# Performance work log

Hardware: AMD Instinct MI355X
Metric: run time of the kernel (lower is better)

The kernel has to match this reference:

```python
import jax, jax.numpy as jnp
import numpy as np

B, N_H, N = 32, 16, 64
R, REP, NUM_CLS = 1024, 1024, 117
NUM_ITER = 2
T_LIS, K_LIS, W_LIS = 8.3, 12.0, 10.0

# static pair indices: x in [0,n_h), y in [0,n), x != y  -> M = N_H*N - N_H
_xx, _yy = np.meshgrid(np.arange(N_H), np.arange(N), indexing='ij')
_mask = _xx != _yy
X_IDX = jnp.asarray(_xx[_mask], dtype=jnp.int32)  # [M]
Y_IDX = jnp.asarray(_yy[_mask], dtype=jnp.int32)  # [M]
M = int(_mask.sum())


def lis(x):
    # low-grade suppression
    return T_LIS / (1.0 + jnp.exp(K_LIS - W_LIS * x))


def setup_inputs() -> dict:
    key = jax.random.key(0)
    ks = jax.random.split(key, 18)
    s = 0.02
    p = lambda k, shp: (jax.random.normal(k, shp) * s).astype(jnp.float32)
    box_features = jax.random.normal(ks[0], (B, N, R), dtype=jnp.float32)
    box_coords = jax.random.uniform(ks[1], (B, N, 4), dtype=jnp.float32)
    box_labels = jax.random.randint(ks[2], (B, N), 0, NUM_CLS).astype(jnp.int32)
    box_labels = box_labels.at[:, :N_H].set(0)  # first N_H are humans (human_idx=0)
    box_scores = jax.random.uniform(ks[3], (B, N), dtype=jnp.float32)
    return {
        'box_features': box_features, 'box_coords': box_coords,
        'box_labels': box_labels, 'box_scores': box_scores,
        'W1': p(ks[4], (2 * R, REP)), 'b1': jnp.zeros((REP,), jnp.float32),
        'W2': p(ks[5], (REP, REP // 2)), 'b2': jnp.zeros((REP // 2,), jnp.float32),
        'W3': p(ks[6], (REP // 2, 1)), 'b3': jnp.zeros((1,), jnp.float32),
        'Ws': p(ks[7], (R, REP)), 'bs': jnp.zeros((REP,), jnp.float32),
        'Wo': p(ks[8], (R, REP)), 'bo': jnp.zeros((REP,), jnp.float32),
        'Wsu': p(ks[9], (R + REP, R)),
        'Wou': p(ks[10], (R + REP, R)),
    }


def reference(box_features, box_coords, box_labels, box_scores,
              W1, b1, W2, b2, W3, b3, Ws, bs, Wo, bo, Wsu, Wou):
    def per_image(enc, coords, labels, scores):
        # enc: [N, R]
        A = jnp.zeros((N_H, N), enc.dtype)
        for _ in range(NUM_ITER):
            pe = jnp.concatenate([enc[X_IDX], enc[Y_IDX]], axis=1)  # [M, 2R]
            h = jax.nn.relu(pe @ W1 + b1)
            h = jax.nn.relu(h @ W2 + b2)
            w = (h @ W3 + b3)[:, 0]  # [M]
            A = jnp.zeros((N_H, N), enc.dtype).at[X_IDX, Y_IDX].set(jax.nn.sigmoid(w))
            msg_h = A @ jax.nn.relu(enc @ Wo + bo)                      # [N_H, REP]
            enc_h = jnp.concatenate([enc[:N_H], msg_h], axis=1) @ Wsu  # [N_H, R]
            enc = enc.at[:N_H].set(enc_h)
            msg_o = A.T @ jax.nn.relu(enc_h @ Ws + bs)                  # [N, REP]
            enc = jnp.concatenate([enc, msg_o], axis=1) @ Wou           # [N, R]
        pair = jnp.concatenate([enc[X_IDX], enc[Y_IDX]], axis=1)  # [M, 2R]
        prod = lis(scores[X_IDX]) * lis(scores[Y_IDX])            # [M]
        # identity object_class_to_target_class: class c -> [c]
        prior = jnp.zeros((M, NUM_CLS), enc.dtype).at[jnp.arange(M), labels[Y_IDX]].set(prod)
        prior = A[X_IDX, Y_IDX][:, None] * prior
        return pair, coords[X_IDX], coords[Y_IDX], prior

    pair, bh, bo_, prior = jax.vmap(per_image)(box_features, box_coords, box_labels, box_scores)
    return (pair.reshape(B * M, 2 * R), bh, bo_, prior.reshape(B * M, NUM_CLS))
```

## Files before the change

kernel.cpp:

```cpp
#include <hip/hip_runtime.h>

#define B_   32
#define N_   64
#define NH   16
#define R_   1024
#define REP  1024
#define M_   1008
#define BM   (B_ * M_)
#define NCLS 117

#define MD_DIRECT 0
#define MD_CC1    2

typedef short bhalf8 __attribute__((ext_vector_type(8)));
typedef float f32x4  __attribute__((ext_vector_type(4)));

typedef __attribute__((address_space(3))) void       lds_t;
typedef const __attribute__((address_space(1))) void gbl_t;
__device__ __forceinline__ void gld16(const void* g, void* l)
{
    __builtin_amdgcn_global_load_lds((gbl_t*)g, (lds_t*)l, 16, 0, 0);
}

__device__ __forceinline__ int xcd_swz(int orig, int q)
{
    return (orig & 7) * q + (orig >> 3);
}

__device__ __forceinline__ unsigned short f2bf(float f)
{
    union { float f; unsigned int u; } x; x.f = f;
    unsigned int r = x.u + 0x7FFFu + ((x.u >> 16) & 1u);
    return (unsigned short)(r >> 16);
}
__device__ __forceinline__ float bf2f(unsigned short u)
{
    union { unsigned int i; float f; } x; x.i = ((unsigned int)u) << 16; return x.f;
}

__device__ __forceinline__ unsigned int addrelu2(unsigned int a, unsigned int b)
{
    union { unsigned int u; float f; } la, ha, lb, hb;
    la.u = a << 16;          ha.u = a & 0xffff0000u;
    lb.u = b << 16;          hb.u = b & 0xffff0000u;
    float lo = fmaxf(la.f + lb.f, 0.f);
    float hi = fmaxf(ha.f + hb.f, 0.f);
    unsigned int r;
    asm("v_cvt_pk_bf16_f32 %0, %1, %2" : "=v"(r) : "v"(lo), "v"(hi));
    return r;
}

__device__ __forceinline__ void wait_vm(int n)
{
    if (n >= 8)      asm volatile("s_waitcnt vmcnt(8)" ::: "memory");
    else if (n == 6) asm volatile("s_waitcnt vmcnt(6)" ::: "memory");
    else if (n == 4) asm volatile("s_waitcnt vmcnt(4)" ::: "memory");
    else if (n == 3) asm volatile("s_waitcnt vmcnt(3)" ::: "memory");
    else if (n == 2) asm volatile("s_waitcnt vmcnt(2)" ::: "memory");
    else             asm volatile("s_waitcnt vmcnt(0)" ::: "memory");
}
__device__ __forceinline__ void wait_vm_lgkm(int n)
{
    if (n >= 12)      asm volatile("s_waitcnt vmcnt(12) lgkmcnt(0)" ::: "memory");
    else if (n >= 10) asm volatile("s_waitcnt vmcnt(10) lgkmcnt(0)" ::: "memory");
    else              asm volatile("s_waitcnt vmcnt(8) lgkmcnt(0)" ::: "memory");
}

__device__ __forceinline__ void tr32(const float* in, unsigned short* out,
                                     int K, int N, int local)
{
    __shared__ float t[32][33];
    int kb = K >> 5;
    int k0 = (local % kb) * 32, n0 = (local / kb) * 32;
    int tx = threadIdx.x & 31, ty = threadIdx.x >> 5;
#pragma unroll
    for (int r = 0; r < 4; ++r)
        t[ty + r * 8][tx] = in[(size_t)(k0 + ty + r * 8) * N + n0 + tx];
    __syncthreads();
#pragma unroll
    for (int r = 0; r < 4; ++r)
        out[(size_t)(n0 + ty + r * 8) * K + k0 + tx] = f2bf(t[tx][ty + r * 8]);
}

__global__ __launch_bounds__(256)
void prep_all(const float* __restrict__ W1, const float* __restrict__ W2,
              const float* __restrict__ Wo, const float* __restrict__ Ws,
              const float* __restrict__ Wsu, const float* __restrict__ Wou,
              const float* __restrict__ bo_, const float* __restrict__ b1_,
              const float* __restrict__ feat,
              unsigned short* __restrict__ Wfused, unsigned short* __restrict__ W2t,
              unsigned short* __restrict__ Wst, unsigned short* __restrict__ Wsut,
              unsigned short* __restrict__ Wout, float* __restrict__ biasFull,
              unsigned short* __restrict__ enc0bf)
{
    int bx = blockIdx.x;
    if      (bx < 1024) tr32(W1 + 1024 * 1024, Wfused,               1024, 1024, bx);
    else if (bx < 2048) tr32(Wo,               Wfused + 1024 * 1024, 1024, 1024, bx - 1024);
    else if (bx < 3072) tr32(W1,               Wfused + 2048 * 1024, 1024, 1024, bx - 2048);
    else if (bx < 3584) tr32(W2,  W2t,  1024, 512,  bx - 3072);
    else if (bx < 4608) tr32(Ws,  Wst,  1024, 1024, bx - 3584);
    else if (bx < 6656) tr32(Wsu, Wsut, 2048, 1024, bx - 4608);
    else if (bx < 8704) tr32(Wou, Wout, 2048, 1024, bx - 6656);
    else if (bx < 8716) {
        int c = (bx - 8704) * 256 + threadIdx.x;
        float v = 0.f;
        if (c >= 2048)      v = b1_[c - 2048];
        else if (c >= 1024) v = bo_[c - 1024];
        biasFull[c] = v;
    } else {
        int i = (bx - 8716) * 256 + threadIdx.x;
        float4 a = ((const float4*)feat)[2 * i];
        float4 b = ((const float4*)feat)[2 * i + 1];
        uint4 o;
        o.x = (unsigned)f2bf(a.x) | ((unsigned)f2bf(a.y) << 16);
        o.y = (unsigned)f2bf(a.z) | ((unsigned)f2bf(a.w) << 16);
        o.z = (unsigned)f2bf(b.x) | ((unsigned)f2bf(b.y) << 16);
        o.w = (unsigned)f2bf(b.z) | ((unsigned)f2bf(b.w) << 16);
        ((uint4*)enc0bf)[i] = o;
    }
}

__global__ __launch_bounds__(256)
void gemm_uvgo(const unsigned short* __restrict__ enc,
               const unsigned short* __restrict__ Wf,
               const float* __restrict__ biasFull, unsigned short* __restrict__ XX)
{
    __shared__ unsigned short As[3][128 * 32];
    __shared__ unsigned short Bs[3][128 * 32];
    const int tid  = threadIdx.x;
    const int lane = tid & 63, wave = tid >> 6;
    const int wm = wave & 1, wn = wave >> 1;
    const int l15 = lane & 15, lk = lane >> 4;
    const int wgid = xcd_swz(blockIdx.x, 48);
    const int row0 = (wgid & 15) * 128, col0 = (wgid >> 4) * 128;
    const int kq = (lane & 3) * 8;

    const unsigned short* pA[2];
    const unsigned short* pB[2];
    int ldsOff[2];
#pragma unroll
    for (int i = 0; i < 2; ++i) {
        int tr = wave * 32 + (lane >> 2) + i * 16;
        pA[i]  = enc + (size_t)(row0 + tr) * 1024 + kq;
        pB[i]  = Wf  + (size_t)(col0 + tr) * 1024 + kq;
        ldsOff[i] = wave * 1024 + i * 512 + lane * 8;
    }

#define STG_UV(slot, k0) do {                          \
        gld16(pA[0] + (k0), &As[slot][ldsOff[0]]);     \
        gld16(pA[1] + (k0), &As[slot][ldsOff[1]]);     \
        gld16(pB[0] + (k0), &Bs[slot][ldsOff[0]]);     \
        gld16(pB[1] + (k0), &Bs[slot][ldsOff[1]]); } while (0)

    f32x4 acc[4][4];
#pragma unroll
    for (int i = 0; i < 4; ++i)
#pragma unroll
    for (int j = 0; j < 4; ++j) acc[i][j] = (f32x4)0.f;

    STG_UV(0, 0);
    STG_UV(1, 32);
    for (int t = 0; t < 32; ++t) {
        const int slot = t % 3;
        if (t + 2 < 32) STG_UV((t + 2) % 3, (t + 2) * 32);
        wait_vm(t < 30 ? 8 : (t == 30 ? 4 : 0));
        __builtin_amdgcn_s_barrier();
        __builtin_amdgcn_sched_barrier(0);
        bhalf8 af[4], bf4[4];
#pragma unroll
        for (int mt = 0; mt < 4; ++mt)
            af[mt] = *(bhalf8*)&As[slot][(wm * 64 + mt * 16 + l15) * 32 + lk * 8];
#pragma unroll
        for (int nt = 0; nt < 4; ++nt)
            bf4[nt] = *(bhalf8*)&Bs[slot][(wn * 64 + nt * 16 + l15) * 32 + lk * 8];
#pragma unroll
        for (int mt = 0; mt < 4; ++mt)
#pragma unroll
        for (int nt = 0; nt < 4; ++nt)
            acc[mt][nt] = __builtin_amdgcn_mfma_f32_16x16x32_bf16(af[mt], bf4[nt],
                                                                  acc[mt][nt], 0, 0, 0);
        __builtin_amdgcn_sched_barrier(0);
        __builtin_amdgcn_s_barrier();
    }
#undef STG_UV

#pragma unroll
    for (int mt = 0; mt < 4; ++mt)
#pragma unroll
    for (int r = 0; r < 4; ++r) {
        int row = row0 + wm * 64 + mt * 16 + lk * 4 + r;
#pragma unroll
        for (int nt = 0; nt < 4; ++nt) {
            int col = col0 + wn * 64 + nt * 16 + l15;
            float v = acc[mt][nt][r] + biasFull[col];
            if ((col >> 10) == 1) v = fmaxf(v, 0.f);
            XX[(size_t)row * 3072 + col] = f2bf(v);
        }
    }
}

__global__ __launch_bounds__(256)
void pair_bf(const unsigned short* __restrict__ XX,
             const unsigned short* __restrict__ W2t, const float* __restrict__ b2,
             const float* __restrict__ W3f, float* __restrict__ wpart)
{
    __shared__ unsigned short As[128 * 32];
    __shared__ unsigned short Bs[3][128 * 32];
    __shared__ float red[2][128];
    const int tid  = threadIdx.x;
    const int lane = tid & 63, wave = tid >> 6;
    const int wm = wave & 1, wn = wave >> 1;
    const int l15 = lane & 15, lk = lane >> 4;
    const int wgid = xcd_swz(blockIdx.x, 126);
    const int cx = wgid & 3, ry = wgid >> 2;
    const int row0 = ry * 128, col0 = cx * 128;

    const int srow = tid >> 1, skh = tid & 1;
    int rg = row0 + srow;
    int b  = rg / M_, m = rg % M_;
    int x  = m / 63, jj = m % 63;
    int y  = jj + (jj >= x ? 1 : 0);
    const unsigned short* Up = XX + ((size_t)(b * 64 + x)) * 3072 + 2048 + skh * 16;
    const unsigned short* Vp = XX + ((size_t)(b * 64 + y)) * 3072 + skh * 16;
    unsigned short* AsW = As + srow * 32 + skh * 16;

    const int kq = (lane & 3) * 8;
    const unsigned short* pB[2];
    int bO[2];
#pragma unroll
    for (int i = 0; i < 2; ++i) {
        int tr = wave * 32 + (lane >> 2) + i * 16;
        pB[i] = W2t + (size_t)(col0 + tr) * REP + kq;
        bO[i] = wave * 1024 + i * 512 + lane * 8;
    }

#define STG_B(slot, k0) do {                        \
        gld16(pB[0] + (k0), &Bs[slot][bO[0]]);      \
        gld16(pB[1] + (k0), &Bs[slot][bO[1]]); } while (0)

    f32x4 acc[4][4];
#pragma unroll
    for (int i = 0; i < 4; ++i)
#pragma unroll
    for (int j = 0; j < 4; ++j) acc[i][j] = (f32x4)0.f;

    uint4 cu0 = *(const uint4*)(Up);
    uint4 cu1 = *(const uint4*)(Up + 8);
    uint4 cv0 = *(const uint4*)(Vp);
    uint4 cv1 = *(const uint4*)(Vp + 8);
    STG_B(0, 0);
    STG_B(1, 32);

    for (int t = 0; t < 32; ++t) {
        const int slot = t % 3;
        const int kn = (t + 1 < 32) ? (t + 1) * 32 : 0;
        uint4 nu0 = *(const uint4*)(Up + kn);
        uint4 nu1 = *(const uint4*)(Up + kn + 8);
        uint4 nv0 = *(const uint4*)(Vp + kn);
        uint4 nv1 = *(const uint4*)(Vp + kn + 8);
        if (t + 2 < 32) STG_B((t + 2) % 3, (t + 2) * 32);

        uint4 h0, h1;
        h0.x = addrelu2(cu0.x, cv0.x); h0.y = addrelu2(cu0.y, cv0.y);
        h0.z = addrelu2(cu0.z, cv0.z); h0.w = addrelu2(cu0.w, cv0.w);
        h1.x = addrelu2(cu1.x, cv1.x); h1.y = addrelu2(cu1.y, cv1.y);
        h1.z = addrelu2(cu1.z, cv1.z); h1.w = addrelu2(cu1.w, cv1.w);
        *(uint4*)(AsW)     = h0;
        *(uint4*)(AsW + 8) = h1;

        wait_vm_lgkm(t == 0 ? 8 : (t < 30 ? 12 : (t == 30 ? 10 : 8)));
        __builtin_amdgcn_s_barrier();
        __builtin_amdgcn_sched_barrier(0);
        bhalf8 af[4], bf4[4];
#pragma unroll
        for (int mt = 0; mt < 4; ++mt)
            af[mt] = *(bhalf8*)&As[(wm * 64 + mt * 16 + l15) * 32 + lk * 8];
#pragma unroll
        for (int nt = 0; nt < 4; ++nt)
            bf4[nt] = *(bhalf8*)&Bs[slot][(wn * 64 + nt * 16 + l15) * 32 + lk * 8];
#pragma unroll
        for (int mt = 0; mt < 4; ++mt)
#pragma unroll
        for (int nt = 0; nt < 4; ++nt)
            acc[mt][nt] = __builtin_amdgcn_mfma_f32_16x16x32_bf16(af[mt], bf4[nt],
                                                                  acc[mt][nt], 0, 0, 0);
        __builtin_amdgcn_sched_barrier(0);
        __builtin_amdgcn_s_barrier();
        cu0 = nu0; cu1 = nu1; cv0 = nv0; cv1 = nv1;
    }
#undef STG_B

    float b2v[4], w3v[4];
#pragma unroll
    for (int nt = 0; nt < 4; ++nt) {
        int col = col0 + wn * 64 + nt * 16 + l15;
        b2v[nt] = b2[col];
        w3v[nt] = W3f[col];
    }
#pragma unroll
    for (int mt = 0; mt < 4; ++mt)
#pragma unroll
    for (int r = 0; r < 4; ++r) {
        int rloc = wm * 64 + mt * 16 + lk * 4 + r;
        float p = 0.f;
#pragma unroll
        for (int nt = 0; nt < 4; ++nt)
            p += fmaxf(acc[mt][nt][r] + b2v[nt], 0.f) * w3v[nt];
        p += __shfl_xor(p, 1); p += __shfl_xor(p, 2);
        p += __shfl_xor(p, 4); p += __shfl_xor(p, 8);
        if (l15 == 0) red[wn][rloc] = p;
    }
    __syncthreads();
    if (tid < 128)
        wpart[cx * BM + row0 + tid] = red[0][tid] + red[1][tid];
}

__device__ __forceinline__ void compute_A(const float* __restrict__ wpart, float b3v,
                                          int b, float* Al, int t)
{
    for (int i = t; i < NH * N_; i += 128) {
        int y = i & 63, x = i >> 6;
        float v = 0.f;
        if (y != x) {
            int j = y - (y > x ? 1 : 0);
            int r = b * M_ + x * 63 + j;
            float s = b3v + wpart[r] + wpart[BM + r] + wpart[2 * BM + r] + wpart[3 * BM + r];
            v = 1.f / (1.f + expf(-s));
        }
        Al[i] = v;
    }
}

__global__ __launch_bounds__(128)
void msgh_kernel(const float* __restrict__ wpart, const float* __restrict__ b3,
                 const unsigned short* __restrict__ XX,
                 unsigned short* __restrict__ msgh)
{
    __shared__ float Al[NH * N_];
    __shared__ float Gl[N_][128];
    const int wgid = xcd_swz(blockIdx.x, 32);
    int b = wgid >> 3, c0 = (wgid & 7) * 128, t = threadIdx.x;
    compute_A(wpart, b3[0], b, Al, t);
    for (int y = 0; y < N_; ++y)
        Gl[y][t] = bf2f(XX[((size_t)(b * 64 + y)) * 3072 + 1024 + c0 + t]);
    __syncthreads();
    for (int x = 0; x < NH; ++x) {
        float s = 0.f;
#pragma unroll 8
        for (int y = 0; y < N_; ++y) s += Al[x * N_ + y] * Gl[y][t];
        msgh[((size_t)(b * NH + x)) * REP + c0 + t] = f2bf(s);
    }
}

__global__ __launch_bounds__(256)
void gemm_small(const unsigned short* __restrict__ A1, const unsigned short* __restrict__ A2,
                const unsigned short* __restrict__ Bt, const float* __restrict__ bias,
                unsigned short* __restrict__ Cb, int K, int Nc, int doRelu, int mode)
{
    __shared__ unsigned short As[4][64 * 32];
    __shared__ unsigned short Bs[4][64 * 32];
    const int tid  = threadIdx.x;
    const int lane = tid & 63, wave = tid >> 6;
    const int wr = wave & 1, wc = wave >> 1;
    const int l15 = lane & 15, lk = lane >> 4;
    const int wgid = xcd_swz(blockIdx.x, 16);
    const int row0 = (wgid & 7) * 64, col0 = (wgid >> 3) * 64;
    const int kq = (lane & 3) * 8;

    int tr = wave * 16 + (lane >> 2);
    int rr = row0 + tr;
    const unsigned short* p1;
    const unsigned short* p2 = nullptr;
    if (mode == MD_DIRECT) {
        p1 = A1 + (size_t)rr * K;
    } else {
        int b = rr >> 4, x = rr & 15;
        p1 = A1 + (size_t)(b * 64 + x) * 1024;
        p2 = A2 + (size_t)rr * 1024 - 1024;
    }
    const unsigned short* pA1 = p1 + kq;
    const unsigned short* pA2 = p2 ? p2 + kq : nullptr;
    const unsigned short* pB  = Bt + (size_t)(col0 + tr) * K + kq;
    const int stO = wave * 512 + lane * 8;
    const int kSw = (mode != MD_DIRECT) ? 1024 : K;
    const int NT = K >> 5;

#define STG_MID(slot, k0) do {                                  \
        const unsigned short* ap = ((k0) < kSw) ? pA1 : pA2;    \
        gld16(ap + (k0), &As[slot][stO]);                       \
        gld16(pB + (k0), &Bs[slot][stO]); } while (0)

    f32x4 acc[2][2];
#pragma unroll
    for (int i = 0; i < 2; ++i)
#pragma unroll
    for (int j = 0; j < 2; ++j) acc[i][j] = (f32x4)0.f;

    STG_MID(0, 0);
    STG_MID(1, 32);
    STG_MID(2, 64);
    for (int t = 0; t < NT; ++t) {
        const int slot = t & 3;
        if (t + 3 < NT) STG_MID((t + 3) & 3, (t + 3) * 32);
        int rem = NT - 1 - t;
        wait_vm(rem >= 3 ? 6 : rem * 2);
        __builtin_amdgcn_s_barrier();
        __builtin_amdgcn_sched_barrier(0);
        bhalf8 af[2], bf4[2];
#pragma unroll
        for (int mt = 0; mt < 2; ++mt)
            af[mt] = *(bhalf8*)&As[slot][(wr * 32 + mt * 16 + l15) * 32 + lk * 8];
#pragma unroll
        for (int nt = 0; nt < 2; ++nt)
            bf4[nt] = *(bhalf8*)&Bs[slot][(wc * 32 + nt * 16 + l15) * 32 + lk * 8];
#pragma unroll
        for (int mt = 0; mt < 2; ++mt)
#pragma unroll
        for (int nt = 0; nt < 2; ++nt)
            acc[mt][nt] = __builtin_amdgcn_mfma_f32_16x16x32_bf16(af[mt], bf4[nt],
                                                                  acc[mt][nt], 0, 0, 0);
        __builtin_amdgcn_sched_barrier(0);
        __builtin_amdgcn_s_barrier();
    }
#undef STG_MID

#pragma unroll
    for (int mt = 0; mt < 2; ++mt)
#pragma unroll
    for (int r = 0; r < 4; ++r) {
        int row = row0 + wr * 32 + mt * 16 + lk * 4 + r;
#pragma unroll
        for (int nt = 0; nt < 2; ++nt) {
            int col = col0 + wc * 32 + nt * 16 + l15;
            float v = acc[mt][nt][r];
            if (bias) v += bias[col];
            if (doRelu) v = fmaxf(v, 0.f);
            Cb[(size_t)row * Nc + col] = f2bf(v);
        }
    }
}

__global__ __launch_bounds__(256)
void gemm_cc2(const unsigned short* __restrict__ enc,
              const unsigned short* __restrict__ ench,
              const unsigned short* __restrict__ Gs,
              const unsigned short* __restrict__ Wout,
              const float* __restrict__ wpart, const float* __restrict__ b3,
              float* __restrict__ Cf, unsigned short* __restrict__ Cb)
{
    __shared__ unsigned short As[3][64 * 32];
    __shared__ unsigned short Bt[3][64 * 32];
    __shared__ unsigned short Bb[3][64 * 32];
    __shared__ unsigned short GsL[16][1056];
    __shared__ float Al[16][64];
    __shared__ float gsl[16][68];

    const int tid  = threadIdx.x;
    const int lane = tid & 63, wave = tid >> 6;
    const int wr = wave & 1, wc = wave >> 1;
    const int l15 = lane & 15, lk = lane >> 4;
    const int wgid = xcd_swz(blockIdx.x, 64);
    const int b = wgid >> 4, col0 = (wgid & 15) * 64;
    const int kq = (lane & 3) * 8;

#pragma unroll
    for (int j = 0; j < 8; ++j) {
        int idx = j * 256 + tid;
        int row = idx >> 7, c8 = (idx & 127) * 8;
        uint4 v = *(const uint4*)(Gs + ((size_t)(b * 16 + row)) * 1024 + c8);
        *(uint4*)&GsL[row][c8] = v;
    }
    float b3v = b3[0];
#pragma unroll
    for (int j = 0; j < 4; ++j) {
        int i = j * 256 + tid;
        int y = i & 63, x = i >> 6;
        float v = 0.f;
        if (y != x) {
            int jj = y - (y > x ? 1 : 0);
            int r = b * M_ + x * 63 + jj;
            float s = b3v + wpart[r] + wpart[BM + r] + wpart[2 * BM + r] + wpart[3 * BM + r];
            v = 1.f / (1.f + expf(-s));
        }
        Al[x][y] = v;
    }
    asm volatile("s_waitcnt lgkmcnt(0)" ::: "memory");

    int tr = wave * 16 + (lane >> 2);
    const unsigned short* pA = (tr < 16 ? ench + ((size_t)(b * 16 + tr)) * 1024
                                        : enc  + ((size_t)(b * 64 + tr)) * 1024) + kq;
    const unsigned short* pBt = Wout + (size_t)(col0 + tr) * 2048 + kq;
    const unsigned short* pBb = pBt + 1024;
    const int stO = wave * 512 + lane * 8;

#define STG_C2(slot, k0) do {                      \
        gld16(pA  + (k0), &As[slot][stO]);         \
        gld16(pBt + (k0), &Bt[slot][stO]);         \
        gld16(pBb + (k0), &Bb[slot][stO]); } while (0)

    f32x4 acc[2][2];
    f32x4 accg[2];
#pragma unroll
    for (int i = 0; i < 2; ++i) {
        accg[i] = (f32x4)0.f;
#pragma unroll
        for (int j = 0; j < 2; ++j) acc[i][j] = (f32x4)0.f;
    }

    STG_C2(0, 0);
    STG_C2(1, 32);
    for (int t = 0; t < 32; ++t) {
        const int slot = t % 3;
        if (t + 2 < 32) STG_C2((t + 2) % 3, (t + 2) * 32);
        wait_vm(t < 30 ? 6 : (t == 30 ? 3 : 0));
        __builtin_amdgcn_s_barrier();
        __builtin_amdgcn_sched_barrier(0);
        bhalf8 af[2], bt4[2], bb4[2], ags;
#pragma unroll
        for (int mt = 0; mt < 2; ++mt)
            af[mt] = *(bhalf8*)&As[slot][(wr * 32 + mt * 16 + l15) * 32 + lk * 8];
#pragma unroll
        for (int nt = 0; nt < 2; ++nt) {
            bt4[nt] = *(bhalf8*)&Bt[slot][(wc * 32 + nt * 16 + l15) * 32 + lk * 8];
            bb4[nt] = *(bhalf8*)&Bb[slot][(wc * 32 + nt * 16 + l15) * 32 + lk * 8];
        }
        ags = *(bhalf8*)&GsL[l15][t * 32 + lk * 8];
#pragma unroll
        for (int mt = 0; mt < 2; ++mt)
#pragma unroll
        for (int nt = 0; nt < 2; ++nt)
            acc[mt][nt] = __builtin_amdgcn_mfma_f32_16x16x32_bf16(af[mt], bt4[nt],
                                                                  acc[mt][nt], 0, 0, 0);
#pragma unroll
        for (int nt = 0; nt < 2; ++nt)
            accg[nt] = __builtin_amdgcn_mfma_f32_16x16x32_bf16(ags, bb4[nt],
                                                               accg[nt], 0, 0, 0);
        __builtin_amdgcn_sched_barrier(0);
        __builtin_amdgcn_s_barrier();
    }
#undef STG_C2

    if (wr == 0) {
#pragma unroll
        for (int nt = 0; nt < 2; ++nt)
#pragma unroll
        for (int r = 0; r < 4; ++r)
            gsl[lk * 4 + r][wc * 32 + nt * 16 + l15] = accg[nt][r];
    }
    __syncthreads();

#pragma unroll
    for (int x = 0; x < 16; ++x) {
        float g0 = gsl[x][wc * 32 + l15];
        float g1 = gsl[x][wc * 32 + 16 + l15];
#pragma unroll
        for (int mt = 0; mt < 2; ++mt)
#pragma unroll
        for (int r = 0; r < 4; ++r) {
            float a = Al[x][wr * 32 + mt * 16 + lk * 4 + r];
            acc[mt][0][r] += a * g0;
            acc[mt][1][r] += a * g1;
        }
    }
#pragma unroll
    for (int mt = 0; mt < 2; ++mt)
#pragma unroll
    for (int r = 0; r < 4; ++r) {
        size_t row = (size_t)b * 64 + wr * 32 + mt * 16 + lk * 4 + r;
#pragma unroll
        for (int nt = 0; nt < 2; ++nt) {
            int col = col0 + wc * 32 + nt * 16 + l15;
            float v = acc[mt][nt][r];
            if (Cf) Cf[row * 1024 + col] = v;
            else    Cb[row * 1024 + col] = f2bf(v);
        }
    }
}

__device__ __forceinline__ float lis_f(float x)
{
    return 8.3f / (1.f + expf(12.f - 10.f * x));
}

__global__ __launch_bounds__(256)
void outputs_all(const float* __restrict__ enc, const float* __restrict__ coords,
                 const float* __restrict__ wpart, const float* __restrict__ b3,
                 const int* __restrict__ labels, const float* __restrict__ scores,
                 float* __restrict__ out0, float* __restrict__ out1,
                 float* __restrict__ out2, float* __restrict__ out3)
{
    int bx = blockIdx.x;
    if (bx < 64512) {
        int i = bx * 256 + threadIdx.x;
        int r = i >> 9, q = i & 511;
        int b = r / M_, m = r % M_;
        int x = m / 63, j = m % 63;
        int y = j + (j >= x ? 1 : 0);
        const float4* e4 = (const float4*)enc;
        float4 v = (q < 256) ? e4[(b * 64 + x) * 256 + q]
                             : e4[(b * 64 + y) * 256 + (q - 256)];
        ((float4*)out0)[i] = v;
    } else if (bx < 64638) {
        int r = (bx - 64512) * 256 + threadIdx.x;
        int b = r / M_, m = r % M_;
        int x = m / 63, j = m % 63;
        int y = j + (j >= x ? 1 : 0);
        const float4* c4 = (const float4*)coords;
        ((float4*)out1)[r] = c4[b * 64 + x];
        ((float4*)out2)[r] = c4[b * 64 + y];
    } else {
        int i = (bx - 64638) * 256 + threadIdx.x;
        int r = i / NCLS, c = i % NCLS;
        int b = r / M_, m = r % M_;
        int x = m / 63, j = m % 63;
        int y = j + (j >= x ? 1 : 0);
        int lab = labels[b * 64 + y];
        float val = 0.f;
        if (c == lab) {
            float w = b3[0] + wpart[r] + wpart[BM + r] + wpart[2 * BM + r] + wpart[3 * BM + r];
            float A = 1.f / (1.f + expf(-w));
            float sx = scores[b * 64 + x], sy = scores[b * 64 + y];
            val = A * lis_f(sx) * lis_f(sy);
        }
        out3[i] = val;
    }
}

extern "C" void kernel_launch(void* const* d_in, const int* in_sizes, int n_in,
                              void* d_out, int out_size, void* d_ws, size_t ws_size,
                              hipStream_t stream)
{
    const float* box_features = (const float*)d_in[0];
    const float* box_coords   = (const float*)d_in[1];
    const int*   box_labels   = (const int*)d_in[2];
    const float* box_scores   = (const float*)d_in[3];
    const float* W1  = (const float*)d_in[4];
    const float* b1  = (const float*)d_in[5];
    const float* W2  = (const float*)d_in[6];
    const float* b2  = (const float*)d_in[7];
    const float* W3  = (const float*)d_in[8];
    const float* b3  = (const float*)d_in[9];
    const float* Ws  = (const float*)d_in[10];
    const float* bs  = (const float*)d_in[11];
    const float* Wo  = (const float*)d_in[12];
    const float* bo  = (const float*)d_in[13];
    const float* Wsu = (const float*)d_in[14];
    const float* Wou = (const float*)d_in[15];

    float* wsf  = (float*)d_ws;
    float* encA = wsf;           wsf += (size_t)B_ * N_ * R_;
    float* wpart= wsf;           wsf += (size_t)4 * BM;
    float* biasFull = wsf;       wsf += 3072;

    unsigned short* wsu = (unsigned short*)wsf;
    unsigned short* enc0bf = wsu;  wsu += (size_t)B_ * N_ * R_;
    unsigned short* encIbf = wsu;  wsu += (size_t)B_ * N_ * R_;
    unsigned short* XX     = wsu;  wsu += (size_t)B_ * N_ * 3072;
    unsigned short* msghbf = wsu;  wsu += (size_t)B_ * NH * REP;
    unsigned short* enchbf = wsu;  wsu += (size_t)B_ * NH * R_;
    unsigned short* Gsbf   = wsu;  wsu += (size_t)B_ * NH * REP;
    unsigned short* Wfused = wsu;  wsu += (size_t)3072 * 1024;
    unsigned short* W2t    = wsu;  wsu += (size_t)512 * 1024;
    unsigned short* Wst    = wsu;  wsu += (size_t)1024 * 1024;
    unsigned short* Wsut   = wsu;  wsu += (size_t)1024 * 2048;
    unsigned short* Wout   = wsu;  wsu += (size_t)1024 * 2048;

    float* out0 = (float*)d_out;
    float* out1 = out0 + (size_t)BM * 2048;
    float* out2 = out1 + (size_t)BM * 4;
    float* out3 = out2 + (size_t)BM * 4;

    prep_all<<<9740, 256, 0, stream>>>(W1, W2, Wo, Ws, Wsu, Wou, bo, b1, box_features,
                                       Wfused, W2t, Wst, Wsut, Wout, biasFull, enc0bf);

    for (int it = 0; it < 2; ++it) {
        const unsigned short* enc = (it == 0) ? enc0bf : encIbf;
        gemm_uvgo<<<384, 256, 0, stream>>>(enc, Wfused, biasFull, XX);
        pair_bf<<<1008, 256, 0, stream>>>(XX, W2t, b2, W3, wpart);
        msgh_kernel<<<256, 128, 0, stream>>>(wpart, b3, XX, msghbf);
        gemm_small<<<128, 256, 0, stream>>>(enc, msghbf, Wsut, nullptr,
                                            enchbf, 2048, 1024, 0, MD_CC1);
        gemm_small<<<128, 256, 0, stream>>>(enchbf, nullptr, Wst, bs,
                                            Gsbf, 1024, 1024, 1, MD_DIRECT);
        gemm_cc2<<<512, 256, 0, stream>>>(enc, enchbf, Gsbf, Wout, wpart, b3,
                                          (it == 1) ? encA : nullptr,
                                          (it == 0) ? encIbf : nullptr);
    }

    outputs_all<<<79380, 256, 0, stream>>>(encA, box_coords, wpart, b3,
                                           box_labels, box_scores,
                                           out0, out1, out2, out3);
}
```

Baseline: 709.8 us.

## Widen pair_bf tiles to full 512 columns, removing split-N partial sums

The pair MLP kernel now has each 512-thread workgroup compute all 512 hidden columns for 128 pair rows, instead of four workgroups each covering 128 columns. The relu(U+V) A-tile is then built once per row block rather than four times, and the four-way wpart partial-sum buffer and its summation in the consumer kernels go away. The trade-off is a larger LDS footprint (about 96KB for B staging), more accumulator registers per thread, and only 252 workgroups, which could lower occupancy and make pipelining less effective on 256 CUs. The XCD swizzle is generalized to handle 252 blocks not dividing evenly by 8.

```diff
diff --git a/kernel.cpp b/kernel.cpp
--- a/kernel.cpp
+++ b/kernel.cpp
@@ -26,6 +26,11 @@
 {
     return (orig & 7) * q + (orig >> 3);
 }
+__device__ __forceinline__ int xcd_swz_gen(int orig, int q, int r)
+{
+    int x = orig & 7, o = orig >> 3;
+    return (x < r ? x * (q + 1) : r * (q + 1) + (x - r) * q) + o;
+}
 
 __device__ __forceinline__ unsigned short f2bf(float f)
 {
@@ -61,9 +66,10 @@
 }
 __device__ __forceinline__ void wait_vm_lgkm(int n)
 {
-    if (n >= 12)      asm volatile("s_waitcnt vmcnt(12) lgkmcnt(0)" ::: "memory");
-    else if (n >= 10) asm volatile("s_waitcnt vmcnt(10) lgkmcnt(0)" ::: "memory");
-    else              asm volatile("s_waitcnt vmcnt(8) lgkmcnt(0)" ::: "memory");
+    if (n >= 10)     asm volatile("s_waitcnt vmcnt(10) lgkmcnt(0)" ::: "memory");
+    else if (n >= 6) asm volatile("s_waitcnt vmcnt(6) lgkmcnt(0)" ::: "memory");
+    else if (n >= 4) asm volatile("s_waitcnt vmcnt(4) lgkmcnt(0)" ::: "memory");
+    else             asm volatile("s_waitcnt vmcnt(0) lgkmcnt(0)" ::: "memory");
 }
 
 __device__ __forceinline__ void tr32(const float* in, unsigned short* out,
@@ -199,101 +205,95 @@
     }
 }
 
-__global__ __launch_bounds__(256)
+__global__ __launch_bounds__(512)
 void pair_bf(const unsigned short* __restrict__ XX,
              const unsigned short* __restrict__ W2t, const float* __restrict__ b2,
              const float* __restrict__ W3f, float* __restrict__ wpart)
 {
     __shared__ unsigned short As[128 * 32];
-    __shared__ unsigned short Bs[3][128 * 32];
-    __shared__ float red[2][128];
+    __shared__ unsigned short Bs[3][512 * 32];
+    __shared__ float red[4][128];
     const int tid  = threadIdx.x;
     const int lane = tid & 63, wave = tid >> 6;
     const int wm = wave & 1, wn = wave >> 1;
     const int l15 = lane & 15, lk = lane >> 4;
-    const int wgid = xcd_swz(blockIdx.x, 126);
-    const int cx = wgid & 3, ry = wgid >> 2;
-    const int row0 = ry * 128, col0 = cx * 128;
-
-    const int srow = tid >> 1, skh = tid & 1;
+    const int wgid = xcd_swz_gen(blockIdx.x, 31, 4);
+    const int row0 = wgid * 128;
+
+    const int srow = tid >> 2, skq = (tid & 3) * 8;
     int rg = row0 + srow;
     int b  = rg / M_, m = rg % M_;
     int x  = m / 63, jj = m % 63;
     int y  = jj + (jj >= x ? 1 : 0);
-    const unsigned short* Up = XX + ((size_t)(b * 64 + x)) * 3072 + 2048 + skh * 16;
-    const unsigned short* Vp = XX + ((size_t)(b * 64 + y)) * 3072 + skh * 16;
-    unsigned short* AsW = As + srow * 32 + skh * 16;
+    const unsigned short* Up = XX + ((size_t)(b * 64 + x)) * 3072 + 2048 + skq;
+    const unsigned short* Vp = XX + ((size_t)(b * 64 + y)) * 3072 + skq;
+    unsigned short* AsW = As + srow * 32 + skq;
 
     const int kq = (lane & 3) * 8;
-    const unsigned short* pB[2];
-    int bO[2];
-#pragma unroll
-    for (int i = 0; i < 2; ++i) {
-        int tr = wave * 32 + (lane >> 2) + i * 16;
-        pB[i] = W2t + (size_t)(col0 + tr) * REP + kq;
-        bO[i] = wave * 1024 + i * 512 + lane * 8;
+    const unsigned short* pB[4];
+    int bO[4];
+#pragma unroll
+    for (int i = 0; i < 4; ++i) {
+        int trB = wave * 64 + i * 16 + (lane >> 2);
+        pB[i] = W2t + (size_t)trB * REP + kq;
+        bO[i] = wave * 2048 + i * 512 + lane * 8;
     }
 
 #define STG_B(slot, k0) do {                        \
         gld16(pB[0] + (k0), &Bs[slot][bO[0]]);      \
-        gld16(pB[1] + (k0), &Bs[slot][bO[1]]); } while (0)
-
-    f32x4 acc[4][4];
+        gld16(pB[1] + (k0), &Bs[slot][bO[1]]);      \
+        gld16(pB[2] + (k0), &Bs[slot][bO[2]]);      \
+        gld16(pB[3] + (k0), &Bs[slot][bO[3]]); } while (0)
+
+    f32x4 acc[4][8];
 #pragma unroll
     for (int i = 0; i < 4; ++i)
 #pragma unroll
-    for (int j = 0; j < 4; ++j) acc[i][j] = (f32x4)0.f;
-
-    uint4 cu0 = *(const uint4*)(Up);
-    uint4 cu1 = *(const uint4*)(Up + 8);
-    uint4 cv0 = *(const uint4*)(Vp);
-    uint4 cv1 = *(const uint4*)(Vp + 8);
+    for (int j = 0; j < 8; ++j) acc[i][j] = (f32x4)0.f;
+
+    uint4 cu = *(const uint4*)(Up);
+    uint4 cv = *(const uint4*)(Vp);
     STG_B(0, 0);
     STG_B(1, 32);
 
     for (int t = 0; t < 32; ++t) {
         const int slot = t % 3;
         const int kn = (t + 1 < 32) ? (t + 1) * 32 : 0;
-        uint4 nu0 = *(const uint4*)(Up + kn);
-        uint4 nu1 = *(const uint4*)(Up + kn + 8);
-        uint4 nv0 = *(const uint4*)(Vp + kn);
-        uint4 nv1 = *(const uint4*)(Vp + kn + 8);
+        uint4 nu = *(const uint4*)(Up + kn);
+        uint4 nv = *(const uint4*)(Vp + kn);
         if (t + 2 < 32) STG_B((t + 2) % 3, (t + 2) * 32);
 
-        uint4 h0, h1;
-        h0.x = addrelu2(cu0.x, cv0.x); h0.y = addrelu2(cu0.y, cv0.y);
-        h0.z = addrelu2(cu0.z, cv0.z); h0.w = addrelu2(cu0.w, cv0.w);
-        h1.x = addrelu2(cu1.x, cv1.x); h1.y = addrelu2(cu1.y, cv1.y);
-        h1.z = addrelu2(cu1.z, cv1.z); h1.w = addrelu2(cu1.w, cv1.w);
-        *(uint4*)(AsW)     = h0;
-        *(uint4*)(AsW + 8) = h1;
-
-        wait_vm_lgkm(t == 0 ? 8 : (t < 30 ? 12 : (t == 30 ? 10 : 8)));
-        __builtin_amdgcn_s_barrier();
-        __builtin_amdgcn_sched_barrier(0);
-        bhalf8 af[4], bf4[4];
+        uint4 h;
+        h.x = addrelu2(cu.x, cv.x); h.y = addrelu2(cu.y, cv.y);
+        h.z = addrelu2(cu.z, cv.z); h.w = addrelu2(cu.w, cv.w);
+        *(uint4*)AsW = h;
+
+        wait_vm_lgkm(t < 30 ? 10 : (t == 30 ? 6 : 4));
+        __builtin_amdgcn_s_barrier();
+        __builtin_amdgcn_sched_barrier(0);
+        bhalf8 af[4], bf4[8];
 #pragma unroll
         for (int mt = 0; mt < 4; ++mt)
             af[mt] = *(bhalf8*)&As[(wm * 64 + mt * 16 + l15) * 32 + lk * 8];
 #pragma unroll
-        for (int nt = 0; nt < 4; ++nt)
-            bf4[nt] = *(bhalf8*)&Bs[slot][(wn * 64 + nt * 16 + l15) * 32 + lk * 8];
+        for (int nt = 0; nt < 8; ++nt)
+            bf4[nt] = *(bhalf8*)&Bs[slot][(wn * 128 + nt * 16 + l15) * 32 + lk * 8];
 #pragma unroll
         for (int mt = 0; mt < 4; ++mt)
 #pragma unroll
-        for (int nt = 0; nt < 4; ++nt)
+        for (int nt = 0; nt < 8; ++nt)
             acc[mt][nt] = __builtin_amdgcn_mfma_f32_16x16x32_bf16(af[mt], bf4[nt],
                                                                   acc[mt][nt], 0, 0, 0);
         __builtin_amdgcn_sched_barrier(0);
         __builtin_amdgcn_s_barrier();
-        cu0 = nu0; cu1 = nu1; cv0 = nv0; cv1 = nv1;
+        cu = nu; cv = nv;
     }
 #undef STG_B
 
-    float b2v[4], w3v[4];
-#pragma unroll
-    for (int nt = 0; nt < 4; ++nt) {
-        int col = col0 + wn * 64 + nt * 16 + l15;
+    float b2v[8], w3v[8];
+#pragma unroll
+    for (int nt = 0; nt < 8; ++nt) {
+        int col = wn * 128 + nt * 16 + l15;
         b2v[nt] = b2[col];
         w3v[nt] = W3f[col];
     }
@@ -304,7 +304,7 @@
         int rloc = wm * 64 + mt * 16 + lk * 4 + r;
         float p = 0.f;
 #pragma unroll
-        for (int nt = 0; nt < 4; ++nt)
+        for (int nt = 0; nt < 8; ++nt)
             p += fmaxf(acc[mt][nt][r] + b2v[nt], 0.f) * w3v[nt];
         p += __shfl_xor(p, 1); p += __shfl_xor(p, 2);
         p += __shfl_xor(p, 4); p += __shfl_xor(p, 8);
@@ -312,7 +312,7 @@
     }
     __syncthreads();
     if (tid < 128)
-        wpart[cx * BM + row0 + tid] = red[0][tid] + red[1][tid];
+        wpart[row0 + tid] = red[0][tid] + red[1][tid] + red[2][tid] + red[3][tid];
 }
 
 __device__ __forceinline__ void compute_A(const float* __restrict__ wpart, float b3v,
@@ -323,8 +323,7 @@
         float v = 0.f;
         if (y != x) {
             int j = y - (y > x ? 1 : 0);
-            int r = b * M_ + x * 63 + j;
-            float s = b3v + wpart[r] + wpart[BM + r] + wpart[2 * BM + r] + wpart[3 * BM + r];
+            float s = b3v + wpart[b * M_ + x * 63 + j];
             v = 1.f / (1.f + expf(-s));
         }
         Al[i] = v;
@@ -478,8 +477,7 @@
         float v = 0.f;
         if (y != x) {
             int jj = y - (y > x ? 1 : 0);
-            int r = b * M_ + x * 63 + jj;
-            float s = b3v + wpart[r] + wpart[BM + r] + wpart[2 * BM + r] + wpart[3 * BM + r];
+            float s = b3v + wpart[b * M_ + x * 63 + jj];
             v = 1.f / (1.f + expf(-s));
         }
         Al[x][y] = v;
@@ -617,7 +615,7 @@
         int lab = labels[b * 64 + y];
         float val = 0.f;
         if (c == lab) {
-            float w = b3[0] + wpart[r] + wpart[BM + r] + wpart[2 * BM + r] + wpart[3 * BM + r];
+            float w = b3[0] + wpart[r];
             float A = 1.f / (1.f + expf(-w));
             float sx = scores[b * 64 + x], sy = scores[b * 64 + y];
             val = A * lis_f(sx) * lis_f(sy);
@@ -649,7 +647,7 @@
 
     float* wsf  = (float*)d_ws;
     float* encA = wsf;           wsf += (size_t)B_ * N_ * R_;
-    float* wpart= wsf;           wsf += (size_t)4 * BM;
+    float* wpart= wsf;           wsf += (size_t)BM;
     float* biasFull = wsf;       wsf += 3072;
 
     unsigned short* wsu = (unsigned short*)wsf;
@@ -676,7 +674,7 @@
     for (int it = 0; it < 2; ++it) {
         const unsigned short* enc = (it == 0) ? enc0bf : encIbf;
         gemm_uvgo<<<384, 256, 0, stream>>>(enc, Wfused, biasFull, XX);
-        pair_bf<<<1008, 256, 0, stream>>>(XX, W2t, b2, W3, wpart);
+        pair_bf<<<252, 512, 0, stream>>>(XX, W2t, b2, W3, wpart);
         msgh_kernel<<<256, 128, 0, stream>>>(wpart, b3, XX, msghbf);
         gemm_small<<<128, 256, 0, stream>>>(enc, msghbf, Wsut, nullptr,
                                             enchbf, 2048, 1024, 0, MD_CC1);
```

New measurement: 663.9 us. -6.5%, faster.
